# Performance work log

Measured on AMD Instinct MI355X. Metric: run time of the kernel, lower is better.

## Reference

```python
import jax, jax.numpy as jnp
import numpy as np

N = 50000      # nodes per side
E = 800000     # edges per side
G = 1024       # graphs per batch
VOCAB = 100000
EMB, GH, EH, OUT = 128, 256, 256, 128
HID = GH + EH


def setup_inputs() -> dict:
    key = jax.random.key(0)
    ks = jax.random.split(key, 32)

    def xav(k, shape):
        lim = float(np.sqrt(6.0 / (shape[0] + shape[1])))
        return jax.random.uniform(k, shape, jnp.float32, -lim, lim)

    inp = {
        "x1": jax.random.randint(ks[0], (N,), 0, 11),
        "edge_index1": jax.random.randint(ks[1], (2, E), 0, N),
        "ent1": jax.random.randint(ks[2], (G,), 0, VOCAB),
        "batch1": jnp.sort(jax.random.randint(ks[3], (N,), 0, G)),
        "x2": jax.random.randint(ks[4], (N,), 0, 11),
        "edge_index2": jax.random.randint(ks[5], (2, E), 0, N),
        "ent2": jax.random.randint(ks[6], (G,), 0, VOCAB),
        "batch2": jnp.sort(jax.random.randint(ks[7], (N,), 0, G)),
        # shared GCN params (xavier weights, zero biases as in _reset_params)
        "atom_emb": xav(ks[8], (11, EMB)),
        "gW1": xav(ks[9], (EMB, GH)), "gb1": jnp.zeros((GH,), jnp.float32),
        "gW2": xav(ks[10], (GH, GH)), "gb2": jnp.zeros((GH,), jnp.float32),
        "fcW": xav(ks[11], (GH, GH)), "fcb": jnp.zeros((GH,), jnp.float32),
        # shared entity encoder params
        "ent_emb": xav(ks[12], (VOCAB, EMB)),
        "eW1": xav(ks[13], (EMB, EH)), "eb1": jnp.zeros((EH,), jnp.float32),
        "eW2": xav(ks[14], (EH, EH)), "eb2": jnp.zeros((EH,), jnp.float32),
        # decoder params
        "dW1": xav(ks[15], (HID, HID)), "db1": jnp.zeros((HID,), jnp.float32),
        "dW2": xav(ks[16], (HID, HID)), "db2": jnp.zeros((HID,), jnp.float32),
        "dW3": xav(ks[17], (HID, OUT)), "db3": jnp.zeros((OUT,), jnp.float32),
    }
    return inp


def _gcn_conv(x, W, b, src, dst, n):
    # PyG GCNConv: self-loops + symmetric normalization, out[dst] += norm * (x@W)[src]
    h = x @ W                                   # [n, d_out]
    loop = jnp.arange(n)
    s = jnp.concatenate([src, loop])
    d = jnp.concatenate([dst, loop])
    deg = jax.ops.segment_sum(jnp.ones_like(s, h.dtype), d, num_segments=n)
    dinv = jnp.where(deg > 0, jax.lax.rsqrt(jnp.maximum(deg, 1e-12)), 0.0)
    norm = dinv[s] * dinv[d]                    # [E+n]
    out = jax.ops.segment_sum(h[s] * norm[:, None], d, num_segments=n)
    return out + b


def _gcn_branch(x, edge_index, batch, atom_emb, gW1, gb1, gW2, gb2, fcW, fcb):
    src, dst = edge_index[0], edge_index[1]
    h = atom_emb[x]                             # [N, EMB]
    h = jax.nn.relu(_gcn_conv(h, gW1, gb1, src, dst, N))
    h = jax.nn.relu(_gcn_conv(h, gW2, gb2, src, dst, N))
    # global mean pool per graph
    counts = jax.ops.segment_sum(jnp.ones((N,), h.dtype), batch, num_segments=G)
    pooled = jax.ops.segment_sum(h, batch, num_segments=G) / jnp.maximum(counts, 1.0)[:, None]
    return pooled @ fcW + fcb                   # [G, GH]


def _enc(ent, ent_emb, eW1, eb1, eW2, eb2):
    e = jax.nn.relu(ent_emb[ent])
    e = jax.nn.relu(e @ eW1 + eb1)
    return jax.nn.relu(e @ eW2 + eb2)           # [G, EH]


def reference(x1, edge_index1, ent1, batch1, x2, edge_index2, ent2, batch2,
              atom_emb, gW1, gb1, gW2, gb2, fcW, fcb,
              ent_emb, eW1, eb1, eW2, eb2,
              dW1, db1, dW2, db2, dW3, db3):
    g1 = _gcn_branch(x1, edge_index1, batch1, atom_emb, gW1, gb1, gW2, gb2, fcW, fcb)
    g2 = _gcn_branch(x2, edge_index2, batch2, atom_emb, gW1, gb1, gW2, gb2, fcW, fcb)
    e1 = _enc(ent1, ent_emb, eW1, eb1, eW2, eb2)
    e2 = _enc(ent2, ent_emb, eW1, eb1, eW2, eb2)
    eg1 = jnp.concatenate([g1, e1], axis=1)     # [G, GH+EH]
    eg2 = jnp.concatenate([g2, e2], axis=1)
    egs = jax.nn.relu(eg1 + eg2)
    h = jax.nn.relu(egs @ dW1 + db1)
    h = jax.nn.relu(h @ dW2 + db2)
    return h @ dW3 + db3                        # [G, OUT]
```

## Files before the change

kernel.cpp:

```cpp
#include <hip/hip_runtime.h>
#include <hip/hip_fp16.h>

static constexpr int kN = 50000;
static constexpr int kE = 800000;
static constexpr int kG = 1024;
static constexpr int kEMB = 128;
static constexpr int kGH = 256;
static constexpr int kEH = 256;
static constexpr int kOUT = 128;
static constexpr int kHID = 512;
static constexpr int kNB = (kN + 255) / 256;
static constexpr int kMD = 64;
static constexpr int kNBKT = 196;
static constexpr int kEPB = 3125;
static constexpr int kPBLK = 256;

typedef __attribute__((ext_vector_type(8))) _Float16 half8v;
typedef __attribute__((ext_vector_type(4))) _Float16 half4v;
typedef __attribute__((ext_vector_type(4))) float floatx4;
typedef __attribute__((ext_vector_type(2))) float floatx2;


#define HS_SCALE 128.0f
#define HS_INV   (1.0f / 128.0f)

__device__ inline void acc_fp8x4(unsigned int w, float& a0, float& a1, float& a2, float& a3) {
    floatx2 lo = __builtin_amdgcn_cvt_pk_f32_fp8(w, false);
    floatx2 hi = __builtin_amdgcn_cvt_pk_f32_fp8(w, true);
    a0 += lo[0]; a1 += lo[1]; a2 += hi[0]; a3 += hi[1];
}

__global__ void setup_kernel(const float* __restrict__ atom_emb, const float* __restrict__ gW1,
                             const float* __restrict__ gW2,
                             float* __restrict__ M11, _Float16* __restrict__ w2t,
                             _Float16* __restrict__ m11t,
                             const float* __restrict__ dW1, const float* __restrict__ dW2,
                             const float* __restrict__ dW3, const float* __restrict__ fcW,
                             const float* __restrict__ eW1, const float* __restrict__ eW2,
                             _Float16* __restrict__ dW1t, _Float16* __restrict__ dW2t,
                             _Float16* __restrict__ dW3t, _Float16* __restrict__ fcWt,
                             _Float16* __restrict__ eW1t, _Float16* __restrict__ eW2t,
                             const int* __restrict__ batch1, const int* __restrict__ batch2,
                             int* __restrict__ gstart) {
    int blk = blockIdx.x;
    int tid = threadIdx.x;
    if (blk < 299) {
        int i = blk * 256 + tid;
        if (blk < 256) {
            int k = i >> 8, n = i & 255;
            w2t[(size_t)n * kGH + k] = (_Float16)gW2[(size_t)k * kGH + n];
        } else {
            int j = i - 65536;
            if (j < 11 * kGH) {
                int r = j >> 8, c = j & 255;
                float s = 0.f;
                for (int k = 0; k < kEMB; k++) s += atom_emb[r * kEMB + k] * gW1[k * kGH + c];
                M11[j] = s;
            } else if (j < 11 * kGH + 256 * 32) {
                int j2 = j - 11 * kGH;
                int n = j2 >> 5, k = j2 & 31;
                float s = 0.f;
                if (k < 11)
                    for (int p = 0; p < kEMB; p++) s += atom_emb[k * kEMB + p] * gW1[p * kGH + n];
                m11t[j2] = (_Float16)s;
            }
        }
    } else if (blk < 299 + 2944) {
        int b = blk - 299;
        const float* src; _Float16* dst; int K, N, j0;
        if (b < 1024)      { src = dW1; dst = dW1t; K = 512; N = 512; j0 = b * 256; }
        else if (b < 2048) { src = dW2; dst = dW2t; K = 512; N = 512; j0 = (b - 1024) * 256; }
        else if (b < 2304) { src = dW3; dst = dW3t; K = 512; N = 128; j0 = (b - 2048) * 256; }
        else if (b < 2560) { src = fcW; dst = fcWt; K = 256; N = 256; j0 = (b - 2304) * 256; }
        else if (b < 2688) { src = eW1; dst = eW1t; K = 128; N = 256; j0 = (b - 2560) * 256; }
        else               { src = eW2; dst = eW2t; K = 256; N = 256; j0 = (b - 2688) * 256; }
        int j = j0 + tid;
        int n = j / K, k = j - n * K;
        dst[j] = (_Float16)src[(size_t)k * N + n];
    } else {
        int b2 = blk - (299 + 2944);
        int side = b2 / 5;
        int g = (b2 % 5) * 256 + tid;
        if (g <= kG) {
            const int* batch = side ? batch2 : batch1;
            int lo = 0, hi = kN;
            while (lo < hi) { int mid = (lo + hi) >> 1; if (batch[mid] < g) lo = mid + 1; else hi = mid; }
            gstart[side * (kG + 1) + g] = lo;
        }
    }
}

__global__ void binp1_kernel(const int* __restrict__ ei1, const int* __restrict__ ei2,
                             int* __restrict__ poff) {
    int side = blockIdx.y;
    const int* dst = (side ? ei2 : ei1) + kE;
    __shared__ int hist[kNBKT];
    int t = threadIdx.x;
    if (t < kNBKT) hist[t] = 0;
    __syncthreads();
    int base = blockIdx.x * kEPB;
    for (int j = t; j < kEPB; j += 256)
        atomicAdd(&hist[dst[base + j] >> 8], 1);
    __syncthreads();
    if (t < kNBKT) poff[((side * kNBKT + t) << 8) | blockIdx.x] = hist[t];
}

__global__ void scanA_kernel(int* __restrict__ poff, int* __restrict__ btot) {
    int b = blockIdx.x, side = blockIdx.y, t = threadIdx.x;
    __shared__ int s[256];
    int idx = ((side * kNBKT + b) << 8) | t;
    int v = poff[idx];
    s[t] = v;
    __syncthreads();
    for (int o = 1; o < 256; o <<= 1) {
        int u = (t >= o) ? s[t - o] : 0;
        __syncthreads();
        s[t] += u;
        __syncthreads();
    }
    poff[idx] = s[t] - v;
    if (t == 255) btot[side * kNBKT + b] = s[255];
}

__launch_bounds__(256)
__global__ void binp2_kernel(const int* __restrict__ ei1, const int* __restrict__ ei2,
                             const int* __restrict__ poff, const int* __restrict__ btot,
                             unsigned int* __restrict__ ebuf) {
    int side = blockIdx.y, blk = blockIdx.x, t = threadIdx.x;
    const int* ei = side ? ei2 : ei1;
    __shared__ int hist[kNBKT], lb[kNBKT], gb[kNBKT], scanbuf[256];
    __shared__ unsigned int sorted[kEPB];
    int bv = (t < kNBKT) ? btot[side * kNBKT + t] : 0;
    scanbuf[t] = bv;
    __syncthreads();
    for (int o = 1; o < 256; o <<= 1) {
        int u = (t >= o) ? scanbuf[t - o] : 0;
        __syncthreads();
        scanbuf[t] += u;
        __syncthreads();
    }
    int gbb = scanbuf[t] - bv;
    __syncthreads();
    if (t < kNBKT) hist[t] = 0;
    __syncthreads();
    int base = blk * kEPB;
    for (int j = t; j < kEPB; j += 256)
        atomicAdd(&hist[ei[kE + base + j] >> 8], 1);
    __syncthreads();
    int v = (t < kNBKT) ? hist[t] : 0;
    scanbuf[t] = v;
    __syncthreads();
    for (int o = 1; o < 256; o <<= 1) {
        int u = (t >= o) ? scanbuf[t - o] : 0;
        __syncthreads();
        scanbuf[t] += u;
        __syncthreads();
    }
    if (t < kNBKT) {
        lb[t] = scanbuf[t] - v;
        gb[t] = gbb + poff[((side * kNBKT + t) << 8) | blk];
        hist[t] = 0;
    }
    __syncthreads();
    for (int j = t; j < kEPB; j += 256) {
        int s_ = ei[base + j];
        int d  = ei[kE + base + j];
        int b  = d >> 8;
        int r  = atomicAdd(&hist[b], 1);
        sorted[lb[b] + r] = ((unsigned int)d << 16) | (unsigned int)s_;
    }
    __syncthreads();
    for (int j = t; j < kEPB; j += 256) {
        unsigned int val = sorted[j];
        int b = val >> 24;
        int gpos = gb[b] + (j - lb[b]);
        ebuf[(size_t)side * kE + gpos] = val;
    }
}

__global__ void binp3_kernel(const unsigned int* __restrict__ ebuf, const int* __restrict__ btot,
                             unsigned short* __restrict__ col_ell, int* __restrict__ counts,
                             float* __restrict__ dinv, int2* __restrict__ xd,
                             const int* __restrict__ x1, const int* __restrict__ x2) {
    int b = blockIdx.x, side = blockIdx.y, t = threadIdx.x;
    __shared__ int s[256];
    __shared__ int cnt[256];
    int bv = (t < kNBKT) ? btot[side * kNBKT + t] : 0;
    s[t] = bv;
    cnt[t] = 0;
    __syncthreads();
    for (int o = 1; o < 256; o <<= 1) {
        int u = (t >= o) ? s[t - o] : 0;
        __syncthreads();
        s[t] += u;
        __syncthreads();
    }
    int start = (b > 0) ? s[b - 1] : 0;
    int end   = s[b];
    for (int k = start + t; k < end; k += 256) {
        unsigned int v = ebuf[(size_t)side * kE + k];
        int d8 = (v >> 16) & 255;
        int slot = atomicAdd(&cnt[d8], 1);
        if (slot > kMD - 1) slot = kMD - 1;
        int node = (b << 8) | d8;
        col_ell[((size_t)side * kN + node) * kMD + slot] = (unsigned short)(v & 0xFFFFu);
    }
    __syncthreads();
    int node = (b << 8) | t;
    if (node < kN) {
        int d = cnt[t];
        counts[side * kN + node] = d;
        float dv = rsqrtf((float)(d + 1));
        dinv[side * kN + node] = dv;
        const int* x = side ? x2 : x1;
        xd[side * kN + node] = make_int2(x[node], __float_as_int(dv));
    }
}

__global__ void binp4_kernel(const unsigned int* __restrict__ ebuf, const int* __restrict__ btot,
                             const int2* __restrict__ xd, _Float16* __restrict__ wt16) {
    int b = blockIdx.x, side = blockIdx.y, t = threadIdx.x;
    const int2* xdb = xd + (size_t)side * kN;
    __shared__ int s[256];
    __shared__ float wtl[256][16];
    int bv = (t < kNBKT) ? btot[side * kNBKT + t] : 0;
    s[t] = bv;
    #pragma unroll
    for (int q = 0; q < 16; q++) wtl[t][q] = 0.f;
    __syncthreads();
    for (int o = 1; o < 256; o <<= 1) {
        int u = (t >= o) ? s[t - o] : 0;
        __syncthreads();
        s[t] += u;
        __syncthreads();
    }
    int start = (b > 0) ? s[b - 1] : 0;
    int end   = s[b];
    for (int k = start + t; k < end; k += 256) {
        unsigned int v = ebuf[(size_t)side * kE + k];
        int src = v & 0xFFFFu;
        int d8 = (v >> 16) & 255;
        int2 xs = xdb[src];
        atomicAdd(&wtl[d8][xs.x], __int_as_float(xs.y));
    }
    __syncthreads();
    int node = (b << 8) | t;
    if (node < kN) {
        int2 xv = xdb[node];
        float dv = __int_as_float(xv.y);
        float dv2 = dv * dv;
        _Float16* wb = wt16 + ((size_t)side * kN + node) * 32;
        half8v o0, o1, z;
        #pragma unroll
        for (int q = 0; q < 8; q++) {
            o0[q] = (_Float16)(dv * wtl[t][q] + ((xv.x == q) ? dv2 : 0.f));
            o1[q] = (_Float16)(dv * wtl[t][q + 8] + ((xv.x == q + 8) ? dv2 : 0.f));
            z[q] = (_Float16)0.f;
        }
        *(half8v*)(wb) = o0;
        *(half8v*)(wb + 8) = o1;
        *(half8v*)(wb + 16) = z;
        *(half8v*)(wb + 24) = z;
    }
}

__launch_bounds__(256)
__global__ void gemm2f_kernel(const _Float16* __restrict__ wt16,
                              const _Float16* __restrict__ m11t,
                              const float* __restrict__ b1,
                              const _Float16* __restrict__ Bt,
                              const float* __restrict__ dinv,
                              unsigned char* __restrict__ C) {
    __shared__ _Float16 As[128][72];
    __shared__ _Float16 Bs[128][72];

    int side = blockIdx.z;
    const _Float16* Aw = wt16 + (size_t)side * kN * 32;
    const float* db = dinv + (size_t)side * kN;
    unsigned char* Cb = C + (size_t)side * kN * kGH;

    int tid = threadIdx.x;
    int wave = tid >> 6, lane = tid & 63;
    int quad = lane >> 4, r = lane & 15;
    int wm = wave >> 1, wn = wave & 1;
    int row0 = blockIdx.x * 128;
    int col0 = blockIdx.y * 128;

    floatx4 acc[4][4];
    #pragma unroll
    for (int i = 0; i < 4; i++)
        #pragma unroll
        for (int j = 0; j < 4; j++) acc[i][j] = (floatx4){0.f, 0.f, 0.f, 0.f};

    half8v afw[2];
    #pragma unroll
    for (int mt = 0; mt < 2; mt++) {
        int gr = row0 + wave * 32 + mt * 16 + r;
        if (gr >= kN) gr = kN - 1;
        afw[mt] = *(const half8v*)(Aw + (size_t)gr * 32 + quad * 8);
    }

    for (int k0 = 0; k0 < kGH; k0 += 64) {
        #pragma unroll
        for (int u = 0; u < 4; u++) {
            int idx = tid + u * 256;
            int row = idx >> 3;
            int seg = (idx & 7) * 8;
            *(half8v*)&Bs[row][seg] = *(const half8v*)(Bt + (size_t)(col0 + row) * kGH + k0 + seg);
        }
        #pragma unroll
        for (int nt = 0; nt < 4; nt++) {
            half8v bfw = *(const half8v*)(m11t + (size_t)(k0 + nt * 16 + r) * 32 + quad * 8);
            float4 bia = *(const float4*)(b1 + k0 + nt * 16 + quad * 4);
            #pragma unroll
            for (int mt = 0; mt < 2; mt++) {
                floatx4 d = (floatx4){0.f, 0.f, 0.f, 0.f};
                d = __builtin_amdgcn_mfma_f32_16x16x32_f16(bfw, afw[mt], d, 0, 0, 0);
                half4v o;
                o[0] = (_Float16)fmaxf(d[0] + bia.x, 0.f);
                o[1] = (_Float16)fmaxf(d[1] + bia.y, 0.f);
                o[2] = (_Float16)fmaxf(d[2] + bia.z, 0.f);
                o[3] = (_Float16)fmaxf(d[3] + bia.w, 0.f);
                *(half4v*)&As[wave * 32 + mt * 16 + r][nt * 16 + quad * 4] = o;
            }
        }
        __syncthreads();
        #pragma unroll
        for (int ks = 0; ks < 2; ks++) {
            half8v af[4], bf[4];
            #pragma unroll
            for (int mt = 0; mt < 4; mt++)
                af[mt] = *(const half8v*)&As[wm * 64 + mt * 16 + r][ks * 32 + quad * 8];
            #pragma unroll
            for (int nt = 0; nt < 4; nt++)
                bf[nt] = *(const half8v*)&Bs[wn * 64 + nt * 16 + r][ks * 32 + quad * 8];
            #pragma unroll
            for (int mt = 0; mt < 4; mt++)
                #pragma unroll
                for (int nt = 0; nt < 4; nt++)
                    acc[mt][nt] = __builtin_amdgcn_mfma_f32_16x16x32_f16(af[mt], bf[nt],
                                                                         acc[mt][nt], 0, 0, 0);
        }
        __syncthreads();
    }

    #pragma unroll
    for (int mt = 0; mt < 4; mt++) {
        #pragma unroll
        for (int i = 0; i < 4; i++) {
            int grow = row0 + wm * 64 + mt * 16 + quad * 4 + i;
            if (grow >= kN) continue;
            float rsq = db[grow] * HS_SCALE;
            #pragma unroll
            for (int nt = 0; nt < 4; nt++) {
                int gcol = col0 + wn * 64 + nt * 16 + r;
                float q = acc[mt][nt][i] * rsq;
                Cb[(size_t)grow * kGH + gcol] =
                    (unsigned char)__builtin_amdgcn_cvt_pk_fp8_f32(q, q, 0, false);
            }
        }
    }
}

__launch_bounds__(256)
__global__ void gemm_tail_kernel(const _Float16* __restrict__ A,
                                 const _Float16* __restrict__ Bt,
                                 void* __restrict__ Cout,
                                 int N, int K,
                                 const float* __restrict__ bias,
                                 int relu, int f32out) {
    __shared__ _Float16 As[64][72];
    __shared__ _Float16 Bs[64][72];
    int tid = threadIdx.x;
    int wave = tid >> 6, lane = tid & 63;
    int quad = lane >> 4, r = lane & 15;
    int wm = wave >> 1, wn = wave & 1;
    int row0 = blockIdx.x * 64, col0 = blockIdx.y * 64;

    floatx4 acc[2][2];
    #pragma unroll
    for (int i = 0; i < 2; i++)
        #pragma unroll
        for (int j = 0; j < 2; j++) acc[i][j] = (floatx4){0.f, 0.f, 0.f, 0.f};

    for (int k0 = 0; k0 < K; k0 += 64) {
        #pragma unroll
        for (int u = 0; u < 2; u++) {
            int idx = tid + u * 256;
            int row = idx >> 3;
            int seg = (idx & 7) * 8;
            *(half8v*)&As[row][seg] = *(const half8v*)(A + (size_t)(row0 + row) * K + k0 + seg);
            *(half8v*)&Bs[row][seg] = *(const half8v*)(Bt + (size_t)(col0 + row) * K + k0 + seg);
        }
        __syncthreads();
        #pragma unroll
        for (int ks = 0; ks < 2; ks++) {
            half8v af[2], bf[2];
            #pragma unroll
            for (int mt = 0; mt < 2; mt++)
                af[mt] = *(const half8v*)&As[wm * 32 + mt * 16 + r][ks * 32 + quad * 8];
            #pragma unroll
            for (int nt = 0; nt < 2; nt++)
                bf[nt] = *(const half8v*)&Bs[wn * 32 + nt * 16 + r][ks * 32 + quad * 8];
            #pragma unroll
            for (int mt = 0; mt < 2; mt++)
                #pragma unroll
                for (int nt = 0; nt < 2; nt++)
                    acc[mt][nt] = __builtin_amdgcn_mfma_f32_16x16x32_f16(af[mt], bf[nt],
                                                                         acc[mt][nt], 0, 0, 0);
        }
        __syncthreads();
    }

    #pragma unroll
    for (int mt = 0; mt < 2; mt++) {
        #pragma unroll
        for (int i = 0; i < 4; i++) {
            int grow = row0 + wm * 32 + mt * 16 + quad * 4 + i;
            #pragma unroll
            for (int nt = 0; nt < 2; nt++) {
                int gcol = col0 + wn * 32 + nt * 16 + r;
                float v = acc[mt][nt][i] + bias[gcol];
                if (relu) v = fmaxf(v, 0.f);
                if (f32out) ((float*)Cout)[(size_t)grow * N + gcol] = v;
                else ((_Float16*)Cout)[(size_t)grow * N + gcol] = (_Float16)v;
            }
        }
    }
}

__launch_bounds__(256)
__global__ void gemm_pair_kernel(const _Float16* __restrict__ pooled16,
                                 const _Float16* __restrict__ fcWt,
                                 _Float16* __restrict__ gfc16,
                                 const float* __restrict__ fcb,
                                 const _Float16* __restrict__ e16,
                                 const _Float16* __restrict__ eW1t,
                                 _Float16* __restrict__ etmp16,
                                 const float* __restrict__ eb1) {
    const _Float16* A; const _Float16* Bt; _Float16* Cout; const float* bias;
    int K, relu;
    if (blockIdx.z == 0) { A = pooled16; Bt = fcWt; Cout = gfc16; bias = fcb; K = kGH; relu = 0; }
    else                 { A = e16; Bt = eW1t; Cout = etmp16; bias = eb1; K = kEMB; relu = 1; }
    const int N = kGH;

    __shared__ _Float16 As[64][72];
    __shared__ _Float16 Bs[64][72];
    int tid = threadIdx.x;
    int wave = tid >> 6, lane = tid & 63;
    int quad = lane >> 4, r = lane & 15;
    int wm = wave >> 1, wn = wave & 1;
    int row0 = blockIdx.x * 64, col0 = blockIdx.y * 64;

    floatx4 acc[2][2];
    #pragma unroll
    for (int i = 0; i < 2; i++)
        #pragma unroll
        for (int j = 0; j < 2; j++) acc[i][j] = (floatx4){0.f, 0.f, 0.f, 0.f};

    for (int k0 = 0; k0 < K; k0 += 64) {
        #pragma unroll
        for (int u = 0; u < 2; u++) {
            int idx = tid + u * 256;
            int row = idx >> 3;
            int seg = (idx & 7) * 8;
            *(half8v*)&As[row][seg] = *(const half8v*)(A + (size_t)(row0 + row) * K + k0 + seg);
            *(half8v*)&Bs[row][seg] = *(const half8v*)(Bt + (size_t)(col0 + row) * K + k0 + seg);
        }
        __syncthreads();
        #pragma unroll
        for (int ks = 0; ks < 2; ks++) {
            half8v af[2], bf[2];
            #pragma unroll
            for (int mt = 0; mt < 2; mt++)
                af[mt] = *(const half8v*)&As[wm * 32 + mt * 16 + r][ks * 32 + quad * 8];
            #pragma unroll
            for (int nt = 0; nt < 2; nt++)
                bf[nt] = *(const half8v*)&Bs[wn * 32 + nt * 16 + r][ks * 32 + quad * 8];
            #pragma unroll
            for (int mt = 0; mt < 2; mt++)
                #pragma unroll
                for (int nt = 0; nt < 2; nt++)
                    acc[mt][nt] = __builtin_amdgcn_mfma_f32_16x16x32_f16(af[mt], bf[nt],
                                                                         acc[mt][nt], 0, 0, 0);
        }
        __syncthreads();
    }

    #pragma unroll
    for (int mt = 0; mt < 2; mt++) {
        #pragma unroll
        for (int i = 0; i < 4; i++) {
            int grow = row0 + wm * 32 + mt * 16 + quad * 4 + i;
            #pragma unroll
            for (int nt = 0; nt < 2; nt++) {
                int gcol = col0 + wn * 32 + nt * 16 + r;
                float v = acc[mt][nt][i] + bias[gcol];
                if (relu) v = fmaxf(v, 0.f);
                Cout[(size_t)grow * N + gcol] = (_Float16)v;
            }
        }
    }
}

__global__ void aggregate2_kernel(const unsigned char* __restrict__ hs, const float* __restrict__ dinv,
                                  const int* __restrict__ counts,
                                  const unsigned short* __restrict__ col_ell,
                                  const float* __restrict__ bias, unsigned char* __restrict__ out) {
    int side = blockIdx.y;
    const unsigned char* hb = hs + (size_t)side * kN * kGH;
    const float* dv_ = dinv + side * kN;
    const int* deg = counts + side * kN;
    const unsigned short* ci = col_ell + (size_t)side * kN * kMD;
    unsigned char* ob = out + (size_t)side * kN * kGH;

    int wave = threadIdx.x >> 6;
    int lane = threadIdx.x & 63;
    int v = blockIdx.x * 4 + wave;
    if (v >= kN) return;
    int c = lane * 4;
    float4 bia = *(const float4*)(bias + c);
    float dv = dv_[v];
    float a0 = 0.f, a1 = 0.f, a2 = 0.f, a3 = 0.f;
    acc_fp8x4(*(const unsigned int*)(hb + (size_t)v * kGH + c), a0, a1, a2, a3);
    int cnt = min(deg[v], kMD);
    int idxl = (lane < cnt) ? (int)ci[(size_t)v * kMD + lane] : 0;
    int j = 0;
    for (; j + 16 <= cnt; j += 16) {
        unsigned int w[16];
        #pragma unroll
        for (int u = 0; u < 16; u++)
            w[u] = *(const unsigned int*)(hb + (size_t)__shfl(idxl, j + u) * kGH + c);
        #pragma unroll
        for (int u = 0; u < 16; u++) acc_fp8x4(w[u], a0, a1, a2, a3);
    }
    for (; j + 8 <= cnt; j += 8) {
        unsigned int w[8];
        #pragma unroll
        for (int u = 0; u < 8; u++)
            w[u] = *(const unsigned int*)(hb + (size_t)__shfl(idxl, j + u) * kGH + c);
        #pragma unroll
        for (int u = 0; u < 8; u++) acc_fp8x4(w[u], a0, a1, a2, a3);
    }
    for (; j < cnt; j++)
        acc_fp8x4(*(const unsigned int*)(hb + (size_t)__shfl(idxl, j) * kGH + c),
                  a0, a1, a2, a3);
    float f = dv * HS_INV;
    float q0 = fmaxf(f * a0 + bia.x, 0.f) * HS_SCALE;
    float q1 = fmaxf(f * a1 + bia.y, 0.f) * HS_SCALE;
    float q2 = fmaxf(f * a2 + bia.z, 0.f) * HS_SCALE;
    float q3 = fmaxf(f * a3 + bia.w, 0.f) * HS_SCALE;
    unsigned int w = __builtin_amdgcn_cvt_pk_fp8_f32(q0, q1, 0, false);
    w = __builtin_amdgcn_cvt_pk_fp8_f32(q2, q3, w, true);
    __builtin_nontemporal_store(w, (unsigned int*)(ob + (size_t)v * kGH + c));
}

__global__ void pooleg_kernel(const unsigned char* __restrict__ h,
                              const int* __restrict__ gstart,
                              _Float16* __restrict__ pooled16,
                              const float* __restrict__ emb,
                              const int* __restrict__ ent1, const int* __restrict__ ent2,
                              _Float16* __restrict__ e16) {
    if (blockIdx.y == 2) {
        int rr = blockIdx.x * 2 + (threadIdx.x >> 7);
        int k = threadIdx.x & 127;
        int idx = (rr < kG) ? ent1[rr] : ent2[rr - kG];
        e16[(size_t)rr * kEMB + k] = (_Float16)fmaxf(emb[(size_t)idx * kEMB + k], 0.f);
        return;
    }
    int side = blockIdx.y;
    int g = blockIdx.x;
    const unsigned char* hb = h + (size_t)side * kN * kGH;
    int start = gstart[side * (kG + 1) + g];
    int end   = gstart[side * (kG + 1) + g + 1];
    int wave = threadIdx.x >> 6, lane = threadIdx.x & 63;
    int c = lane * 4;
    float a0 = 0.f, a1 = 0.f, a2 = 0.f, a3 = 0.f;
    for (int v = start + wave; v < end; v += 4)
        acc_fp8x4(*(const unsigned int*)(hb + (size_t)v * kGH + c), a0, a1, a2, a3);
    __shared__ float ps[4][256];
    *(float4*)&ps[wave][c] = make_float4(a0, a1, a2, a3);
    __syncthreads();
    int t = threadIdx.x;
    float s = ps[0][t] + ps[1][t] + ps[2][t] + ps[3][t];
    float inv = HS_INV / fmaxf((float)(end - start), 1.0f);
    pooled16[(size_t)(side * kG + g) * kGH + t] = (_Float16)(s * inv);
}

__global__ void egsprep_kernel(const _Float16* __restrict__ gfc16,
                               const _Float16* __restrict__ ento16,
                               _Float16* __restrict__ egs16) {
    int idx = blockIdx.x * 256 + threadIdx.x;
    int g = idx >> 6;
    int k8 = (idx & 63) * 8;
    const _Float16* src = (k8 < kGH) ? gfc16 : ento16;
    int kk = (k8 < kGH) ? k8 : k8 - kGH;
    half8v a = *(const half8v*)(src + (size_t)g * kGH + kk);
    half8v b = *(const half8v*)(src + (size_t)(g + kG) * kGH + kk);
    half8v o;
    #pragma unroll
    for (int u = 0; u < 8; u++) o[u] = (_Float16)fmaxf((float)a[u] + (float)b[u], 0.f);
    *(half8v*)(egs16 + (size_t)g * kHID + k8) = o;
}

static inline char* carve(char*& p, size_t bytes) {
    char* r = p;
    p += (bytes + 255) & ~(size_t)255;
    return r;
}

extern "C" void kernel_launch(void* const* d_in, const int* in_sizes, int n_in,
                              void* d_out, int out_size, void* d_ws, size_t ws_size,
                              hipStream_t stream) {
    const int*   x1       = (const int*)d_in[0];
    const int*   ei1      = (const int*)d_in[1];
    const int*   ent1     = (const int*)d_in[2];
    const int*   batch1   = (const int*)d_in[3];
    const int*   x2       = (const int*)d_in[4];
    const int*   ei2      = (const int*)d_in[5];
    const int*   ent2     = (const int*)d_in[6];
    const int*   batch2   = (const int*)d_in[7];
    const float* atom_emb = (const float*)d_in[8];
    const float* gW1      = (const float*)d_in[9];
    const float* gb1      = (const float*)d_in[10];
    const float* gW2      = (const float*)d_in[11];
    const float* gb2      = (const float*)d_in[12];
    const float* fcW      = (const float*)d_in[13];
    const float* fcb      = (const float*)d_in[14];
    const float* ent_emb  = (const float*)d_in[15];
    const float* eW1      = (const float*)d_in[16];
    const float* eb1      = (const float*)d_in[17];
    const float* eW2      = (const float*)d_in[18];
    const float* eb2      = (const float*)d_in[19];
    const float* dW1      = (const float*)d_in[20];
    const float* db1      = (const float*)d_in[21];
    const float* dW2      = (const float*)d_in[22];
    const float* db2      = (const float*)d_in[23];
    const float* dW3      = (const float*)d_in[24];
    const float* db3      = (const float*)d_in[25];
    float* out = (float*)d_out;

    char* p = (char*)d_ws;
    unsigned char* h4_8 = (unsigned char*)carve(p, (size_t)2 * kN * kGH);
    unsigned char* hs8  = (unsigned char*)carve(p, (size_t)2 * kN * kGH);
    unsigned short* col_ell = (unsigned short*)carve(p, (size_t)2 * kN * kMD * 2);
    unsigned int* ebuf = (unsigned int*)carve(p, (size_t)2 * kE * 4);
    int*   poff    = (int*)  carve(p, (size_t)2 * kNBKT * 256 * 4);
    int*   btot    = (int*)  carve(p, (size_t)2 * kNBKT * 4);
    int*   counts  = (int*)  carve(p, (size_t)2 * kN * 4);
    float* dinv    = (float*)carve(p, (size_t)2 * kN * 4);
    int2*  xd      = (int2*) carve(p, (size_t)2 * kN * 8);
    int*   gstart  = (int*)  carve(p, (size_t)2 * (kG + 1) * 4);
    float* M11     = (float*)carve(p, 11 * kGH * 4);
    _Float16* w2t  = (_Float16*)carve(p, (size_t)kGH * kGH * 2);
    _Float16* m11t = (_Float16*)carve(p, (size_t)256 * 32 * 2);
    _Float16* wt16 = (_Float16*)carve(p, (size_t)2 * kN * 32 * 2);
    _Float16* pooled16 = (_Float16*)carve(p, (size_t)2 * kG * kGH * 2);
    _Float16* gfc16    = (_Float16*)carve(p, (size_t)2 * kG * kGH * 2);
    _Float16* e16      = (_Float16*)carve(p, (size_t)2 * kG * kEMB * 2);
    _Float16* etmp16   = (_Float16*)carve(p, (size_t)2 * kG * kEH * 2);
    _Float16* ento16   = (_Float16*)carve(p, (size_t)2 * kG * kEH * 2);
    _Float16* egs16    = (_Float16*)carve(p, (size_t)kG * kHID * 2);
    _Float16* dh1_16   = (_Float16*)carve(p, (size_t)kG * kHID * 2);
    _Float16* dh2_16   = (_Float16*)carve(p, (size_t)kG * kHID * 2);
    _Float16* dW1t = (_Float16*)carve(p, (size_t)kHID * kHID * 2);
    _Float16* dW2t = (_Float16*)carve(p, (size_t)kHID * kHID * 2);
    _Float16* dW3t = (_Float16*)carve(p, (size_t)kOUT * kHID * 2);
    _Float16* fcWt = (_Float16*)carve(p, (size_t)kGH * kGH * 2);
    _Float16* eW1t = (_Float16*)carve(p, (size_t)kEH * kEMB * 2);
    _Float16* eW2t = (_Float16*)carve(p, (size_t)kEH * kEH * 2);

    setup_kernel<<<299 + 2944 + 10, 256, 0, stream>>>(
        atom_emb, gW1, gW2, M11, w2t, m11t,
        dW1, dW2, dW3, fcW, eW1, eW2,
        dW1t, dW2t, dW3t, fcWt, eW1t, eW2t,
        batch1, batch2, gstart);
    binp1_kernel<<<dim3(kPBLK, 2), 256, 0, stream>>>(ei1, ei2, poff);
    scanA_kernel<<<dim3(kNBKT, 2), 256, 0, stream>>>(poff, btot);
    binp2_kernel<<<dim3(kPBLK, 2), 256, 0, stream>>>(ei1, ei2, poff, btot, ebuf);
    binp3_kernel<<<dim3(kNBKT, 2), 256, 0, stream>>>(ebuf, btot, col_ell, counts,
                                                     dinv, xd, x1, x2);
    binp4_kernel<<<dim3(kNBKT, 2), 256, 0, stream>>>(ebuf, btot, xd, wt16);
    gemm2f_kernel<<<dim3((kN + 127) / 128, kGH / 128, 2), 256, 0, stream>>>(
        wt16, m11t, gb1, w2t, dinv, hs8);
    aggregate2_kernel<<<dim3((kN + 3) / 4, 2), 256, 0, stream>>>(hs8, dinv, counts, col_ell,
                                                                 gb2, h4_8);
    pooleg_kernel<<<dim3(kG, 3), 256, 0, stream>>>(h4_8, gstart, pooled16,
                                                   ent_emb, ent1, ent2, e16);
    gemm_pair_kernel<<<dim3(2 * kG / 64, kGH / 64, 2), 256, 0, stream>>>(
        pooled16, fcWt, gfc16, fcb, e16, eW1t, etmp16, eb1);
    gemm_tail_kernel<<<dim3(2 * kG / 64, kEH / 64), 256, 0, stream>>>(
        etmp16, eW2t, ento16, kEH, kEH, eb2, 1, 0);
    egsprep_kernel<<<kG * kHID / 8 / 256, 256, 0, stream>>>(gfc16, ento16, egs16);
    gemm_tail_kernel<<<dim3(kG / 64, kHID / 64), 256, 0, stream>>>(
        egs16, dW1t, dh1_16, kHID, kHID, db1, 1, 0);
    gemm_tail_kernel<<<dim3(kG / 64, kHID / 64), 256, 0, stream>>>(
        dh1_16, dW2t, dh2_16, kHID, kHID, db2, 1, 0);
    gemm_tail_kernel<<<dim3(kG / 64, kOUT / 64), 256, 0, stream>>>(
        dh2_16, dW3t, out, kOUT, kHID, db3, 0, 1);
}
```

Measured before the change: 367.6 us.

## Tile weight transposes, fold edge histogram into setup, fuse egs prep into GEMM

The weight transposes in setup now go through a 64x64 shared-memory tile, so both the reads and the writes are coalesced, replacing the old per-element strided gather. The binp1 histogram pass moves into the setup kernel as extra blocks, which removes one launch. The egsprep elementwise kernel is removed and its add+relu of the two branches is done inside the first decoder GEMM's A-tile load, avoiding the egs16 round-trip through memory and another launch. The cost is a bigger setup kernel that needs more shared memory, plus recomputing the add for each column block.

```diff
diff --git a/kernel.cpp b/kernel.cpp
--- a/kernel.cpp
+++ b/kernel.cpp
@@ -41,7 +41,11 @@
                              _Float16* __restrict__ dW3t, _Float16* __restrict__ fcWt,
                              _Float16* __restrict__ eW1t, _Float16* __restrict__ eW2t,
                              const int* __restrict__ batch1, const int* __restrict__ batch2,
-                             int* __restrict__ gstart) {
+                             int* __restrict__ gstart,
+                             const int* __restrict__ ei1, const int* __restrict__ ei2,
+                             int* __restrict__ poff) {
+    __shared__ _Float16 tile[64][66];
+    __shared__ int hist[kNBKT];
     int blk = blockIdx.x;
     int tid = threadIdx.x;
     if (blk < 299) {
@@ -65,20 +69,45 @@
                 m11t[j2] = (_Float16)s;
             }
         }
-    } else if (blk < 299 + 2944) {
+    } else if (blk < 299 + 184) {
         int b = blk - 299;
-        const float* src; _Float16* dst; int K, N, j0;
-        if (b < 1024)      { src = dW1; dst = dW1t; K = 512; N = 512; j0 = b * 256; }
-        else if (b < 2048) { src = dW2; dst = dW2t; K = 512; N = 512; j0 = (b - 1024) * 256; }
-        else if (b < 2304) { src = dW3; dst = dW3t; K = 512; N = 128; j0 = (b - 2048) * 256; }
-        else if (b < 2560) { src = fcW; dst = fcWt; K = 256; N = 256; j0 = (b - 2304) * 256; }
-        else if (b < 2688) { src = eW1; dst = eW1t; K = 128; N = 256; j0 = (b - 2560) * 256; }
-        else               { src = eW2; dst = eW2t; K = 256; N = 256; j0 = (b - 2688) * 256; }
-        int j = j0 + tid;
-        int n = j / K, k = j - n * K;
-        dst[j] = (_Float16)src[(size_t)k * N + n];
+        const float* src; _Float16* dst; int K, N, tt;
+        if (b < 64)       { src = dW1; dst = dW1t; K = 512; N = 512; tt = b; }
+        else if (b < 128) { src = dW2; dst = dW2t; K = 512; N = 512; tt = b - 64; }
+        else if (b < 144) { src = dW3; dst = dW3t; K = 512; N = 128; tt = b - 128; }
+        else if (b < 160) { src = fcW; dst = fcWt; K = 256; N = 256; tt = b - 144; }
+        else if (b < 168) { src = eW1; dst = eW1t; K = 128; N = 256; tt = b - 160; }
+        else              { src = eW2; dst = eW2t; K = 256; N = 256; tt = b - 168; }
+        int tilesN = N >> 6;
+        int tk = tt / tilesN, tn = tt - tk * tilesN;
+        int k0 = tk * 64, n0 = tn * 64;
+        #pragma unroll
+        for (int it = 0; it < 16; it++) {
+            int idx = tid + it * 256;
+            int kk = idx >> 6, nn = idx & 63;
+            tile[kk][nn] = (_Float16)src[(size_t)(k0 + kk) * N + n0 + nn];
+        }
+        __syncthreads();
+        #pragma unroll
+        for (int it = 0; it < 16; it++) {
+            int idx = tid + it * 256;
+            int nn = idx >> 6, kk = idx & 63;
+            dst[(size_t)(n0 + nn) * K + k0 + kk] = tile[kk][nn];
+        }
+    } else if (blk < 299 + 184 + 512) {
+        int b = blk - (299 + 184);
+        int side = b >> 8;
+        int bb = b & 255;
+        const int* dstp = (side ? ei2 : ei1) + kE;
+        if (tid < kNBKT) hist[tid] = 0;
+        __syncthreads();
+        int base = bb * kEPB;
+        for (int j = tid; j < kEPB; j += 256)
+            atomicAdd(&hist[dstp[base + j] >> 8], 1);
+        __syncthreads();
+        if (tid < kNBKT) poff[((side * kNBKT + tid) << 8) | bb] = hist[tid];
     } else {
-        int b2 = blk - (299 + 2944);
+        int b2 = blk - (299 + 184 + 512);
         int side = b2 / 5;
         int g = (b2 % 5) * 256 + tid;
         if (g <= kG) {
@@ -88,21 +117,6 @@
             gstart[side * (kG + 1) + g] = lo;
         }
     }
-}
-
-__global__ void binp1_kernel(const int* __restrict__ ei1, const int* __restrict__ ei2,
-                             int* __restrict__ poff) {
-    int side = blockIdx.y;
-    const int* dst = (side ? ei2 : ei1) + kE;
-    __shared__ int hist[kNBKT];
-    int t = threadIdx.x;
-    if (t < kNBKT) hist[t] = 0;
-    __syncthreads();
-    int base = blockIdx.x * kEPB;
-    for (int j = t; j < kEPB; j += 256)
-        atomicAdd(&hist[dst[base + j] >> 8], 1);
-    __syncthreads();
-    if (t < kNBKT) poff[((side * kNBKT + t) << 8) | blockIdx.x] = hist[t];
 }
 
 __global__ void scanA_kernel(int* __restrict__ poff, int* __restrict__ btot) {
@@ -430,6 +444,81 @@
 }
 
 __launch_bounds__(256)
+__global__ void gemm_egs16_kernel(const _Float16* __restrict__ gfc16,
+                                  const _Float16* __restrict__ ento16,
+                                  const _Float16* __restrict__ Bt,
+                                  _Float16* __restrict__ Cout,
+                                  const float* __restrict__ bias) {
+    const int N = kHID, K = kHID;
+    __shared__ _Float16 As[64][72];
+    __shared__ _Float16 Bs[64][72];
+    int tid = threadIdx.x;
+    int wave = tid >> 6, lane = tid & 63;
+    int quad = lane >> 4, r = lane & 15;
+    int wm = wave >> 1, wn = wave & 1;
+    int row0 = blockIdx.x * 64, col0 = blockIdx.y * 64;
+
+    floatx4 acc[2][2];
+    #pragma unroll
+    for (int i = 0; i < 2; i++)
+        #pragma unroll
+        for (int j = 0; j < 2; j++) acc[i][j] = (floatx4){0.f, 0.f, 0.f, 0.f};
+
+    for (int k0 = 0; k0 < K; k0 += 64) {
+        #pragma unroll
+        for (int u = 0; u < 2; u++) {
+            int idx = tid + u * 256;
+            int row = idx >> 3;
+            int seg = (idx & 7) * 8;
+            int g = row0 + row;
+            int k = k0 + seg;
+            const _Float16* src = (k < kGH) ? gfc16 : ento16;
+            int kk = (k < kGH) ? k : k - kGH;
+            half8v a = *(const half8v*)(src + (size_t)g * kGH + kk);
+            half8v b = *(const half8v*)(src + (size_t)(g + kG) * kGH + kk);
+            half8v o;
+            #pragma unroll
+            for (int q = 0; q < 8; q++)
+                o[q] = (_Float16)fmaxf((float)a[q] + (float)b[q], 0.f);
+            *(half8v*)&As[row][seg] = o;
+            *(half8v*)&Bs[row][seg] = *(const half8v*)(Bt + (size_t)(col0 + row) * K + k0 + seg);
+        }
+        __syncthreads();
+        #pragma unroll
+        for (int ks = 0; ks < 2; ks++) {
+            half8v af[2], bf[2];
+            #pragma unroll
+            for (int mt = 0; mt < 2; mt++)
+                af[mt] = *(const half8v*)&As[wm * 32 + mt * 16 + r][ks * 32 + quad * 8];
+            #pragma unroll
+            for (int nt = 0; nt < 2; nt++)
+                bf[nt] = *(const half8v*)&Bs[wn * 32 + nt * 16 + r][ks * 32 + quad * 8];
+            #pragma unroll
+            for (int mt = 0; mt < 2; mt++)
+                #pragma unroll
+                for (int nt = 0; nt < 2; nt++)
+                    acc[mt][nt] = __builtin_amdgcn_mfma_f32_16x16x32_f16(af[mt], bf[nt],
+                                                                         acc[mt][nt], 0, 0, 0);
+        }
+        __syncthreads();
+    }
+
+    #pragma unroll
+    for (int mt = 0; mt < 2; mt++) {
+        #pragma unroll
+        for (int i = 0; i < 4; i++) {
+            int grow = row0 + wm * 32 + mt * 16 + quad * 4 + i;
+            #pragma unroll
+            for (int nt = 0; nt < 2; nt++) {
+                int gcol = col0 + wn * 32 + nt * 16 + r;
+                float v = fmaxf(acc[mt][nt][i] + bias[gcol], 0.f);
+                Cout[(size_t)grow * N + gcol] = (_Float16)v;
+            }
+        }
+    }
+}
+
+__launch_bounds__(256)
 __global__ void gemm_pair_kernel(const _Float16* __restrict__ pooled16,
                                  const _Float16* __restrict__ fcWt,
                                  _Float16* __restrict__ gfc16,
@@ -585,22 +674,6 @@
     float s = ps[0][t] + ps[1][t] + ps[2][t] + ps[3][t];
     float inv = HS_INV / fmaxf((float)(end - start), 1.0f);
     pooled16[(size_t)(side * kG + g) * kGH + t] = (_Float16)(s * inv);
-}
-
-__global__ void egsprep_kernel(const _Float16* __restrict__ gfc16,
-                               const _Float16* __restrict__ ento16,
-                               _Float16* __restrict__ egs16) {
-    int idx = blockIdx.x * 256 + threadIdx.x;
-    int g = idx >> 6;
-    int k8 = (idx & 63) * 8;
-    const _Float16* src = (k8 < kGH) ? gfc16 : ento16;
-    int kk = (k8 < kGH) ? k8 : k8 - kGH;
-    half8v a = *(const half8v*)(src + (size_t)g * kGH + kk);
-    half8v b = *(const half8v*)(src + (size_t)(g + kG) * kGH + kk);
-    half8v o;
-    #pragma unroll
-    for (int u = 0; u < 8; u++) o[u] = (_Float16)fmaxf((float)a[u] + (float)b[u], 0.f);
-    *(half8v*)(egs16 + (size_t)g * kHID + k8) = o;
 }
 
 static inline char* carve(char*& p, size_t bytes) {
@@ -660,7 +733,6 @@
     _Float16* e16      = (_Float16*)carve(p, (size_t)2 * kG * kEMB * 2);
     _Float16* etmp16   = (_Float16*)carve(p, (size_t)2 * kG * kEH * 2);
     _Float16* ento16   = (_Float16*)carve(p, (size_t)2 * kG * kEH * 2);
-    _Float16* egs16    = (_Float16*)carve(p, (size_t)kG * kHID * 2);
     _Float16* dh1_16   = (_Float16*)carve(p, (size_t)kG * kHID * 2);
     _Float16* dh2_16   = (_Float16*)carve(p, (size_t)kG * kHID * 2);
     _Float16* dW1t = (_Float16*)carve(p, (size_t)kHID * kHID * 2);
@@ -670,12 +742,12 @@
     _Float16* eW1t = (_Float16*)carve(p, (size_t)kEH * kEMB * 2);
     _Float16* eW2t = (_Float16*)carve(p, (size_t)kEH * kEH * 2);
 
-    setup_kernel<<<299 + 2944 + 10, 256, 0, stream>>>(
+    setup_kernel<<<299 + 184 + 512 + 10, 256, 0, stream>>>(
         atom_emb, gW1, gW2, M11, w2t, m11t,
         dW1, dW2, dW3, fcW, eW1, eW2,
         dW1t, dW2t, dW3t, fcWt, eW1t, eW2t,
-        batch1, batch2, gstart);
-    binp1_kernel<<<dim3(kPBLK, 2), 256, 0, stream>>>(ei1, ei2, poff);
+        batch1, batch2, gstart,
+        ei1, ei2, poff);
     scanA_kernel<<<dim3(kNBKT, 2), 256, 0, stream>>>(poff, btot);
     binp2_kernel<<<dim3(kPBLK, 2), 256, 0, stream>>>(ei1, ei2, poff, btot, ebuf);
     binp3_kernel<<<dim3(kNBKT, 2), 256, 0, stream>>>(ebuf, btot, col_ell, counts,
@@ -691,9 +763,8 @@
         pooled16, fcWt, gfc16, fcb, e16, eW1t, etmp16, eb1);
     gemm_tail_kernel<<<dim3(2 * kG / 64, kEH / 64), 256, 0, stream>>>(
         etmp16, eW2t, ento16, kEH, kEH, eb2, 1, 0);
-    egsprep_kernel<<<kG * kHID / 8 / 256, 256, 0, stream>>>(gfc16, ento16, egs16);
-    gemm_tail_kernel<<<dim3(kG / 64, kHID / 64), 256, 0, stream>>>(
-        egs16, dW1t, dh1_16, kHID, kHID, db1, 1, 0);
+    gemm_egs16_kernel<<<dim3(kG / 64, kHID / 64), 256, 0, stream>>>(
+        gfc16, ento16, dW1t, dh1_16, db1);
     gemm_tail_kernel<<<dim3(kG / 64, kHID / 64), 256, 0, stream>>>(
         dh1_16, dW2t, dh2_16, kHID, kHID, db2, 1, 0);
     gemm_tail_kernel<<<dim3(kG / 64, kOUT / 64), 256, 0, stream>>>(
```

Result: no change. 362.9 us (-1.3%).
